# Kernel optimization log

Measured on AMD Instinct MI355X. Metric: run time of the kernel, lower is better.

Reference implementation:

```python
import jax, jax.numpy as jnp
import numpy as np
import math

B, NX, NY = 4, 64, 64
IN_DIM, OUT_DIM = 3, 3
DIM, DEPTH, HEADS, DH, FF_MULT = 192, 6, 8, 64, 4
INNER = HEADS * DH              # 512
FF = DIM * FF_MULT              # 768
M = int(DH * math.log(DH))      # 266 random features (performer default)
GROUPS = 8
LATENT_STEPS = 1
EPS_SN, EPS_K, EPS_GN = 1e-5, 1e-4, 1e-5


def setup_inputs() -> dict:
    rng = np.random.default_rng(0)
    f = lambda *s: jnp.asarray(rng.standard_normal(s).astype(np.float32) * 0.02)
    # unitary forward operator (SVD-whitened in torch == orthogonal matrix)
    Q, _ = np.linalg.qr(rng.standard_normal((DIM, DIM)).astype(np.float32))
    return {
        "x": jnp.asarray(rng.standard_normal((B, NX, NY, IN_DIM)).astype(np.float32)),
        "to_in_w": f(DIM, IN_DIM), "to_in_b": f(DIM),
        "pos_emb": f(1, NX * NY, DIM),
        "proj": jnp.asarray(rng.standard_normal((DEPTH, M, DH)).astype(np.float32)),
        "sn_attn_g": jnp.ones((DEPTH,), jnp.float32),
        "wq": f(DEPTH, INNER, DIM), "wk": f(DEPTH, INNER, DIM), "wv": f(DEPTH, INNER, DIM),
        "wo": f(DEPTH, DIM, INNER), "bo": f(DEPTH, DIM),
        "sn_ff_g": jnp.ones((DEPTH,), jnp.float32),
        "w1": f(DEPTH, FF, DIM), "b1": f(DEPTH, FF),
        "w2": f(DEPTH, DIM, FF), "b2": f(DEPTH, DIM),
        "expand_w": f(DIM, DIM),
        "fwd_w": jnp.asarray(Q.astype(np.float32)),
        "dec_lin_w": f(DIM, DIM), "dec_lin_b": f(DIM),
        "gn_g": jnp.ones((DIM,), jnp.float32), "gn_b": jnp.zeros((DIM,), jnp.float32),
        "c9_w": f(DIM, DIM // GROUPS, 9, 9), "c9_b": f(DIM),
        "c7_w": f(DIM // 2, DIM // GROUPS, 7, 7), "c7_b": f(DIM // 2),
        "c5_w": f(DIM // 4, (DIM // 2) // GROUPS, 5, 5), "c5_b": f(DIM // 4),
        "c1_w": f(OUT_DIM, DIM // 4, 1, 1), "c1_b": f(OUT_DIM),
        "latent_steps": LATENT_STEPS,
    }


def _scalenorm(x, g):
    n = jnp.linalg.norm(x, axis=-1, keepdims=True) * (x.shape[-1] ** -0.5)
    return x / jnp.maximum(n, EPS_SN) * g


def _softmax_features(data, proj, is_query):
    # data: [b,h,n,d]; proj: [m,d] -> FAVOR+ softmax-kernel features [b,h,n,m]
    dn = data.shape[-1] ** -0.25
    ratio = proj.shape[0] ** -0.5
    dd = jnp.einsum('bhnd,md->bhnm', data * dn, proj)
    diag = 0.5 * jnp.sum(data * data, -1) * (dn * dn)  # [b,h,n]
    if is_query:
        mx = jnp.max(dd, axis=-1, keepdims=True)
    else:
        mx = jnp.max(dd, axis=(-1, -2), keepdims=True)
    return ratio * (jnp.exp(dd - diag[..., None] - mx) + EPS_K)


def _attn(x, proj, wq, wk, wv, wo, bo):
    b, n, _ = x.shape
    split = lambda t: t.reshape(b, n, HEADS, DH).transpose(0, 2, 1, 3)
    q = split(x @ wq.T); k = split(x @ wk.T); v = split(x @ wv.T)
    qp = _softmax_features(q, proj, True)
    kp = _softmax_features(k, proj, False)
    context = jnp.einsum('bhnm,bhnd->bhmd', kp, v)            # [b,h,m,d]
    denom = jnp.einsum('bhnm,bhm->bhn', qp, kp.sum(2))
    out = jnp.einsum('bhnm,bhmd->bhnd', qp, context) / denom[..., None]
    out = out.transpose(0, 2, 1, 3).reshape(b, n, INNER)
    return out @ wo.T + bo


def _circ_conv(x, w, b, groups):
    p = w.shape[-1] // 2
    x = jnp.pad(x, ((0, 0), (0, 0), (p, p), (p, p)), mode='wrap')
    y = jax.lax.conv_general_dilated(x, w, (1, 1), 'VALID',
        dimension_numbers=('NCHW', 'OIHW', 'NCHW'), feature_group_count=groups)
    return y + b[None, :, None, None]


def _group_norm(x, g, b):
    B_, C, H, W = x.shape
    xg = x.reshape(B_, GROUPS, C // GROUPS, H, W)
    mu = xg.mean((2, 3, 4), keepdims=True)
    var = xg.var((2, 3, 4), keepdims=True)
    xn = ((xg - mu) * jax.lax.rsqrt(var + EPS_GN)).reshape(B_, C, H, W)
    return xn * g[None, :, None, None] + b[None, :, None, None]


def reference(x, to_in_w, to_in_b, pos_emb, proj, sn_attn_g, wq, wk, wv, wo, bo,
              sn_ff_g, w1, b1, w2, b2, expand_w, fwd_w, dec_lin_w, dec_lin_b,
              gn_g, gn_b, c9_w, c9_b, c7_w, c7_b, c5_w, c5_b, c1_w, c1_b, latent_steps):
    b, nx, ny, _ = x.shape
    h = x @ to_in_w.T + to_in_b                       # [b,nx,ny,dim]
    h = h.reshape(b, nx * ny, DIM) + pos_emb[:, :nx * ny]
    for i in range(DEPTH):                             # Performer: prenorm attn + prenorm FF
        h = h + _attn(_scalenorm(h, sn_attn_g[i]), proj[i], wq[i], wk[i], wv[i], wo[i], bo[i])
        hn = _scalenorm(h, sn_ff_g[i])
        h = h + (jax.nn.gelu(hn @ w1[i].T + b1[i], approximate=False) @ w2[i].T + b2[i])
    h = h.reshape(b, nx, ny, DIM) @ expand_w.T        # expand_latent (no bias)
    u, us = h, []
    for _ in range(latent_steps):
        u = u @ fwd_w.T                               # unitary forward operator
        us.append(u)
    u = jnp.concatenate(us, 0)                        # [(b*t), nx, ny, c]
    y = u @ dec_lin_w.T + dec_lin_b
    y = y.transpose(0, 3, 1, 2)                       # NCHW
    y = _group_norm(y, gn_g, gn_b)
    y = jax.nn.gelu(_circ_conv(y, c9_w, c9_b, GROUPS), approximate=False)
    y = jax.nn.gelu(_circ_conv(y, c7_w, c7_b, GROUPS), approximate=False)
    y = jax.nn.gelu(_circ_conv(y, c5_w, c5_b, GROUPS), approximate=False)
    y = jax.lax.conv_general_dilated(y, c1_w, (1, 1), 'VALID',
        dimension_numbers=('NCHW', 'OIHW', 'NCHW')) + c1_b[None, :, None, None]
    # einops '(b t) c nx ny -> b t nx ny c'
    y = y.reshape(b, latent_steps, OUT_DIM, nx, ny).transpose(0, 1, 3, 4, 2)
    return y
```

## Files before the change

### kernel.cpp

```cpp
#include <hip/hip_runtime.h>
#include <cmath>

#define NB      4
#define NTOK    4096
#define BNTOK   16384
#define CDIM    192
#define CINNER  512
#define NHEADS  8
#define DHEAD   64
#define CFF     768
#define MFEAT   266
#define NDEPTH  6

#define DN      0.35355339059327373f
#define RATIO   0.06131393394849658f

typedef unsigned short u16;
typedef __attribute__((ext_vector_type(8))) short s16x8;
typedef __attribute__((ext_vector_type(8))) u16  u16x8;
typedef __attribute__((ext_vector_type(4))) float f32x4;

#define OFF_H    0ull
#define OFF_HN   3145728ull
#define OFF_Q    6291456ull
#define OFF_K    14680064ull
#define OFF_V    23068672ull
#define OFF_BIG  31457280ull
#define OFF_PJ   44040192ull
#define OFF_CTXT 44163072ull
#define OFF_KMAX 47368192ull
#define OFF_GNP  47368448ull
#define OFF_GNS  47369472ull
#define OFF_WHI  47370240ull
#define OFF_WLO  49489920ull
#define WOFF_QKV 0ull
#define WOFF_WO  1769472ull
#define WOFF_W1  2359296ull
#define WOFF_W2  3244032ull
#define WOFF_EXP 4128768ull
#define WOFF_FWD 4165632ull
#define WOFF_DEC 4202496ull

#define PJL      20480
#define CTXTN    819200

__device__ __forceinline__ float gelu_f(float x) {
    return 0.5f * x * (1.0f + erff(x * 0.7071067811865476f));
}
__device__ __forceinline__ unsigned f2ord(float f) {
    int i = __float_as_int(f);
    return (i >= 0) ? ((unsigned)i | 0x80000000u) : (unsigned)(~i);
}
__device__ __forceinline__ float ord2f(unsigned u) {
    int i = (u & 0x80000000u) ? (int)(u & 0x7fffffffu) : ~(int)u;
    return __int_as_float(i);
}
__device__ __forceinline__ void split_bf16(float a, u16& h, u16& l) {
    unsigned ua = __float_as_uint(a);
    unsigned rh = (ua + 0x7FFFu + ((ua >> 16) & 1u)) >> 16;
    h = (u16)rh;
    float hf = __uint_as_float(rh << 16);
    float lo = a - hf;
    unsigned ul = __float_as_uint(lo);
    unsigned rl = (ul + 0x7FFFu + ((ul >> 16) & 1u)) >> 16;
    l = (u16)rl;
}
__device__ __forceinline__ u16 hi_bf16(float a) {
    unsigned ua = __float_as_uint(a);
    return (u16)((ua + 0x7FFFu + ((ua >> 16) & 1u)) >> 16);
}

__global__ __launch_bounds__(256) void cvt_qkv(const float* __restrict__ wq,
    const float* __restrict__ wk, const float* __restrict__ wv,
    u16* __restrict__ hi, u16* __restrict__ lo)
{
    int idx = blockIdx.x * 256 + threadIdx.x;
    int l = idx / 294912, rem = idx - l * 294912;
    int r = rem / 192, c = rem - r * 192;
    float v;
    if (r < 512)       v = wq[((size_t)l * 512 + r) * 192 + c];
    else if (r < 1024) v = wk[((size_t)l * 512 + (r - 512)) * 192 + c];
    else               v = wv[((size_t)l * 512 + (r - 1024)) * 192 + c];
    u16 h, lw; split_bf16(v, h, lw);
    hi[idx] = h; lo[idx] = lw;
}

__global__ __launch_bounds__(256) void cvt_w(const float* __restrict__ src,
    u16* __restrict__ hi, u16* __restrict__ lo, int n)
{
    int idx = blockIdx.x * 256 + threadIdx.x;
    if (idx < n) {
        u16 h, l; split_bf16(src[idx], h, l);
        hi[idx] = h; lo[idx] = l;
    }
}

__global__ __launch_bounds__(256) void cvt_dec(const float* __restrict__ e,
    const float* __restrict__ f, const float* __restrict__ d,
    u16* __restrict__ hi, u16* __restrict__ lo)
{
    int idx = blockIdx.x * 256 + threadIdx.x;
    if (idx >= 110592) return;
    int which = idx / 36864, rem = idx - which * 36864;
    float v = (which == 0) ? e[rem] : (which == 1) ? f[rem] : d[rem];
    u16 h, l; split_bf16(v, h, l);
    hi[idx] = h; lo[idx] = l;
}

__global__ __launch_bounds__(256) void cvt_pj(const float* __restrict__ proj,
    u16* __restrict__ hi, u16* __restrict__ lo)
{
    int idx = blockIdx.x * 256 + threadIdx.x;
    int l = idx / PJL, rem = idx - l * PJL;
    int m = rem >> 6, k = rem & 63;
    float v = (m < MFEAT) ? proj[(size_t)l * MFEAT * DHEAD + m * 64 + k] : 0.f;
    u16 h, lw; split_bf16(v, h, lw);
    hi[idx] = h; lo[idx] = lw;
}

__global__ __launch_bounds__(256) void input_embed(const float* __restrict__ x,
    const float* __restrict__ w, const float* __restrict__ bvec,
    const float* __restrict__ pos, float* __restrict__ h)
{
    int idx = blockIdx.x * 256 + threadIdx.x;
    int row = idx / CDIM, c = idx - row * CDIM;
    int p = row & (NTOK - 1);
    const float* xr = x + (size_t)row * 3;
    h[idx] = xr[0]*w[c*3+0] + xr[1]*w[c*3+1] + xr[2]*w[c*3+2] + bvec[c] + pos[(size_t)p*CDIM + c];
}

__global__ __launch_bounds__(256) void rownorm_kernel(const float* __restrict__ in,
    float* __restrict__ sv, const float* __restrict__ gptr, int gidx)
{
    int wv = threadIdx.x >> 6, lane = threadIdx.x & 63;
    int row = blockIdx.x * 4 + wv;
    const float* p = in + (size_t)row * CDIM;
    float x0 = p[lane], x1 = p[lane + 64], x2 = p[lane + 128];
    float ss = x0*x0 + x1*x1 + x2*x2;
    #pragma unroll
    for (int off = 32; off; off >>= 1) ss += __shfl_xor(ss, off);
    if (lane == 0) {
        float g = gptr[gidx];
        float n = sqrtf(ss * (1.0f / 192.0f));
        sv[row] = g / fmaxf(n, 1e-5f);
    }
}

#define LP 40
__global__ __launch_bounds__(256) void gemm_mfma(const float* __restrict__ A,
    const float* __restrict__ ascale,
    const u16* __restrict__ Bhi, const u16* __restrict__ Blo,
    const float* __restrict__ bias, const float* __restrict__ resid,
    float* __restrict__ C, int M, int N, int K, int epi)
{
    __shared__ u16 a_hi[128 * LP], a_lo[128 * LP], b_hi[128 * LP], b_lo[128 * LP];
    const int tid = threadIdx.x;
    const int n0 = blockIdx.x * 128, m0 = blockIdx.y * 128;
    const int wave = tid >> 6, lane = tid & 63;
    const int wr = wave >> 1, wc = wave & 1;
    const int fr = lane & 15, q = lane >> 4;
    const bool wactive = (n0 + wc * 64) < N;
    f32x4 acc[4][4];
    #pragma unroll
    for (int i = 0; i < 4; ++i)
        #pragma unroll
        for (int j = 0; j < 4; ++j) { acc[i][j][0]=0.f; acc[i][j][1]=0.f; acc[i][j][2]=0.f; acc[i][j][3]=0.f; }

    const int srow = tid >> 1, sc0 = (tid & 1) * 16;
    const float* aptr = A + (size_t)(m0 + srow) * K + sc0;
    const float as = ascale ? ascale[m0 + srow] : 1.0f;
    const bool bval = (n0 + srow) < N;
    const u16* bhp = Bhi + (size_t)(n0 + srow) * K + sc0;
    const u16* blp = Blo + (size_t)(n0 + srow) * K + sc0;
    const int soff = srow * LP + sc0;
    const int aoffb = (wr * 64 + fr) * LP + q * 8;
    const int boffb = (wc * 64 + fr) * LP + q * 8;

    for (int kc = 0; kc < K; kc += 32) {
        float4 f0 = *(const float4*)(aptr + kc);
        float4 f1 = *(const float4*)(aptr + kc + 4);
        float4 f2 = *(const float4*)(aptr + kc + 8);
        float4 f3 = *(const float4*)(aptr + kc + 12);
        u16x8 h0, l0, h1, l1;
        {
            float v[16] = {f0.x,f0.y,f0.z,f0.w, f1.x,f1.y,f1.z,f1.w,
                           f2.x,f2.y,f2.z,f2.w, f3.x,f3.y,f3.z,f3.w};
            u16 hh[16], ll[16];
            #pragma unroll
            for (int i = 0; i < 16; ++i) { float sv = v[i] * as; split_bf16(sv, hh[i], ll[i]); }
            #pragma unroll
            for (int i = 0; i < 8; ++i) { h0[i]=hh[i]; l0[i]=ll[i]; h1[i]=hh[8+i]; l1[i]=ll[8+i]; }
        }
        *(u16x8*)&a_hi[soff]     = h0;  *(u16x8*)&a_hi[soff + 8] = h1;
        *(u16x8*)&a_lo[soff]     = l0;  *(u16x8*)&a_lo[soff + 8] = l1;
        u16x8 bh0 = (u16x8)0, bh1 = (u16x8)0, bl0 = (u16x8)0, bl1 = (u16x8)0;
        if (bval) {
            bh0 = *(const u16x8*)(bhp + kc);  bh1 = *(const u16x8*)(bhp + kc + 8);
            bl0 = *(const u16x8*)(blp + kc);  bl1 = *(const u16x8*)(blp + kc + 8);
        }
        *(u16x8*)&b_hi[soff]     = bh0;  *(u16x8*)&b_hi[soff + 8] = bh1;
        *(u16x8*)&b_lo[soff]     = bl0;  *(u16x8*)&b_lo[soff + 8] = bl1;
        __syncthreads();
        if (wactive) {
            s16x8 Ah[4], Al[4], Bh[4], Bl[4];
            #pragma unroll
            for (int t = 0; t < 4; ++t) {
                Ah[t] = *(const s16x8*)&a_hi[aoffb + t * 16 * LP];
                Al[t] = *(const s16x8*)&a_lo[aoffb + t * 16 * LP];
                Bh[t] = *(const s16x8*)&b_hi[boffb + t * 16 * LP];
                Bl[t] = *(const s16x8*)&b_lo[boffb + t * 16 * LP];
            }
            #pragma unroll
            for (int i = 0; i < 4; ++i)
                #pragma unroll
                for (int j = 0; j < 4; ++j)
                    acc[i][j] = __builtin_amdgcn_mfma_f32_16x16x32_bf16(Ah[i], Bh[j], acc[i][j], 0, 0, 0);
            #pragma unroll
            for (int i = 0; i < 4; ++i)
                #pragma unroll
                for (int j = 0; j < 4; ++j)
                    acc[i][j] = __builtin_amdgcn_mfma_f32_16x16x32_bf16(Ah[i], Bl[j], acc[i][j], 0, 0, 0);
            #pragma unroll
            for (int i = 0; i < 4; ++i)
                #pragma unroll
                for (int j = 0; j < 4; ++j)
                    acc[i][j] = __builtin_amdgcn_mfma_f32_16x16x32_bf16(Al[i], Bh[j], acc[i][j], 0, 0, 0);
        }
        __syncthreads();
    }
    const int c0 = n0 + wc * 64;
    const int rowb = m0 + wr * 64;
    #pragma unroll
    for (int j = 0; j < 4; ++j) {
        int c = c0 + j * 16 + fr;
        if (c >= N) continue;
        float bb = (epi & 1) ? bias[c] : 0.f;
        float* cp;
        if (epi & 8) cp = C + (size_t)(c >> 9) * 8388608ull + (size_t)(c & 511);
        else         cp = C + c;
        const float* rp = (epi & 4) ? (resid + c) : nullptr;
        #pragma unroll
        for (int i = 0; i < 4; ++i) {
            #pragma unroll
            for (int r = 0; r < 4; ++r) {
                int row = rowb + i * 16 + q * 4 + r;
                float val = acc[i][j][r] + bb;
                if (epi & 2) val = gelu_f(val);
                if (epi & 4) val += rp[(size_t)row * N];
                size_t off = (epi & 8) ? (size_t)row * 512 : (size_t)row * N;
                cp[off] = val;
            }
        }
    }
}

__global__ void kmax_init(unsigned* kmaxu) {
    if (threadIdx.x < NDEPTH * 32) kmaxu[threadIdx.x] = 0u;
}

__global__ __launch_bounds__(256) void kmax2_kernel(const float* __restrict__ Km,
    const u16* __restrict__ pjh, unsigned* __restrict__ kmaxu)
{
    __shared__ __align__(16) u16 khi[64 * 72];
    __shared__ float wred[4];
    const int tid = threadIdx.x;
    const int nt = blockIdx.x, bh = blockIdx.y;
    const int b = bh >> 3, hh = bh & 7;
    const int wave = tid >> 6, lane = tid & 63;
    const int fr = lane & 15, quad = lane >> 4;
    float lm = -1e30f;
    const size_t kbase = ((size_t)b * NTOK) * CINNER + hh * DHEAD;
    for (int ch = 0; ch < 4; ++ch) {
        const int n0 = nt * 256 + ch * 64;
        __syncthreads();
        {
            int tok = tid >> 2, koff = (tid & 3) * 16;
            const float* kp = Km + kbase + (size_t)(n0 + tok) * CINNER + koff;
            u16 hh16[16];
            #pragma unroll
            for (int qd = 0; qd < 4; ++qd) {
                float4 f = *(const float4*)(kp + qd * 4);
                hh16[qd*4+0] = hi_bf16(f.x * DN); hh16[qd*4+1] = hi_bf16(f.y * DN);
                hh16[qd*4+2] = hi_bf16(f.z * DN); hh16[qd*4+3] = hi_bf16(f.w * DN);
            }
            u16x8 v0, v1;
            #pragma unroll
            for (int i = 0; i < 8; ++i) { v0[i] = hh16[i]; v1[i] = hh16[8+i]; }
            *(u16x8*)&khi[tok * 72 + koff] = v0;
            *(u16x8*)&khi[tok * 72 + koff + 8] = v1;
        }
        __syncthreads();
        int rowA = (wave * 16 + fr) * 72;
        s16x8 A0 = *(const s16x8*)&khi[rowA + quad * 8];
        s16x8 A1 = *(const s16x8*)&khi[rowA + 32 + quad * 8];
        for (int ct = 0; ct < 17; ++ct) {
            const u16* bp = pjh + (ct * 16 + fr) * 64 + quad * 8;
            s16x8 B0 = *(const s16x8*)bp;
            s16x8 B1 = *(const s16x8*)(bp + 32);
            f32x4 t; t[0]=0.f; t[1]=0.f; t[2]=0.f; t[3]=0.f;
            t = __builtin_amdgcn_mfma_f32_16x16x32_bf16(A0, B0, t, 0, 0, 0);
            t = __builtin_amdgcn_mfma_f32_16x16x32_bf16(A1, B1, t, 0, 0, 0);
            if (ct * 16 + fr < MFEAT) {
                #pragma unroll
                for (int r = 0; r < 4; ++r) lm = fmaxf(lm, t[r]);
            }
        }
    }
    #pragma unroll
    for (int off = 32; off; off >>= 1) lm = fmaxf(lm, __shfl_xor(lm, off));
    if (lane == 0) wred[wave] = lm;
    __syncthreads();
    if (tid == 0) {
        float m = fmaxf(fmaxf(wred[0], wred[1]), fmaxf(wred[2], wred[3]));
        atomicMax(kmaxu + bh, f2ord(m));
    }
}

__global__ __launch_bounds__(256) void ctx2_kernel(const float* __restrict__ Km,
    const float* __restrict__ Vm, const u16* __restrict__ pjh, const u16* __restrict__ pjl,
    const unsigned* __restrict__ kmaxu, float* __restrict__ part)
{
    __shared__ __align__(16) u16 khi[32 * 72], klo[32 * 72];
    __shared__ __align__(16) u16 vth[80 * 40], vtl[80 * 40];
    __shared__ __align__(16) u16 kph[4][16 * 40], kpl[4][16 * 40];
    __shared__ float diag[32];
    const int tid = threadIdx.x;
    const int bh = blockIdx.x, seg = blockIdx.y;
    const int b = bh >> 3, hh = bh & 7;
    const int wave = tid >> 6, lane = tid & 63;
    const int fr = lane & 15, quad = lane >> 4;
    const float kmx = ord2f(kmaxu[bh]);
    for (int i = tid; i < 16 * 40; i += 256) {
        int row = 64 + i / 40, col = i - (i / 40) * 40;
// ... 30 lines not shown
            #pragma unroll
            for (int i = 0; i < 8; ++i) {
                u16 h, l; split_bf16(vv[i], h, l);
                vth[(koff + i) * 40 + tok] = h;
                vtl[(koff + i) * 40 + tok] = l;
            }
        }
        __syncthreads();
        s16x8 Ah[2][2], Al[2][2];
        #pragma unroll
        for (int rt = 0; rt < 2; ++rt) {
            int rowA = (rt * 16 + fr) * 72;
            Ah[rt][0] = *(const s16x8*)&khi[rowA + quad * 8];
            Ah[rt][1] = *(const s16x8*)&khi[rowA + 32 + quad * 8];
            Al[rt][0] = *(const s16x8*)&klo[rowA + quad * 8];
            Al[rt][1] = *(const s16x8*)&klo[rowA + 32 + quad * 8];
        }
        for (int mc = 0; mc < 5; ++mc) {
            const int ct = mc * 4 + wave;
            const u16* bph = pjh + (ct * 16 + fr) * 64 + quad * 8;
            const u16* bpl = pjl + (ct * 16 + fr) * 64 + quad * 8;
            s16x8 B0h = *(const s16x8*)bph, B1h = *(const s16x8*)(bph + 32);
            s16x8 B0l = *(const s16x8*)bpl, B1l = *(const s16x8*)(bpl + 32);
            const bool valid = (ct * 16 + fr) < MFEAT;
            #pragma unroll
            for (int rt = 0; rt < 2; ++rt) {
                f32x4 dd; dd[0]=0.f; dd[1]=0.f; dd[2]=0.f; dd[3]=0.f;
                dd = __builtin_amdgcn_mfma_f32_16x16x32_bf16(Ah[rt][0], B0h, dd, 0, 0, 0);
                dd = __builtin_amdgcn_mfma_f32_16x16x32_bf16(Ah[rt][0], B0l, dd, 0, 0, 0);
                dd = __builtin_amdgcn_mfma_f32_16x16x32_bf16(Al[rt][0], B0h, dd, 0, 0, 0);
                dd = __builtin_amdgcn_mfma_f32_16x16x32_bf16(Ah[rt][1], B1h, dd, 0, 0, 0);
                dd = __builtin_amdgcn_mfma_f32_16x16x32_bf16(Ah[rt][1], B1l, dd, 0, 0, 0);
                dd = __builtin_amdgcn_mfma_f32_16x16x32_bf16(Al[rt][1], B1h, dd, 0, 0, 0);
                ushort4 ph, pl;
                #pragma unroll
                for (int r = 0; r < 4; ++r) {
                    float dgv = diag[rt * 16 + quad * 4 + r];
                    float val = valid ? RATIO * (expf(dd[r] - dgv - kmx) + 1e-4f) : 0.f;
                    u16 h, l; split_bf16(val, h, l);
                    (&ph.x)[r] = h; (&pl.x)[r] = l;
                }
                *(ushort4*)&sh[fr * 40 + rt * 16 + quad * 4] = ph;
                *(ushort4*)&sl[fr * 40 + rt * 16 + quad * 4] = pl;
            }
            s16x8 Bh = *(const s16x8*)&sh[fr * 40 + quad * 8];
            s16x8 Bl = *(const s16x8*)&sl[fr * 40 + quad * 8];
            #pragma unroll
            for (int rt2 = 0; rt2 < 5; ++rt2) {
                s16x8 Vh = *(const s16x8*)&vth[(rt2 * 16 + fr) * 40 + quad * 8];
                s16x8 Vl = *(const s16x8*)&vtl[(rt2 * 16 + fr) * 40 + quad * 8];
                accv[rt2][mc] = __builtin_amdgcn_mfma_f32_16x16x32_bf16(Vh, Bh, accv[rt2][mc], 0, 0, 0);
                accv[rt2][mc] = __builtin_amdgcn_mfma_f32_16x16x32_bf16(Vh, Bl, accv[rt2][mc], 0, 0, 0);
                accv[rt2][mc] = __builtin_amdgcn_mfma_f32_16x16x32_bf16(Vl, Bh, accv[rt2][mc], 0, 0, 0);
            }
        }
    }
    float* pb = part + ((size_t)(seg * 32 + bh)) * 80 * 320;
    #pragma unroll
    for (int rt2 = 0; rt2 < 5; ++rt2) {
        #pragma unroll
        for (int mc = 0; mc < 5; ++mc) {
            int ct = mc * 4 + wave;
            #pragma unroll
            for (int r = 0; r < 4; ++r)
                pb[(size_t)(rt2 * 16 + quad * 4 + r) * 320 + ct * 16 + fr] = accv[rt2][mc][r];
        }
    }
}

__global__ __launch_bounds__(256) void ctxt_reduce(const float* __restrict__ part,
    u16* __restrict__ cth, u16* __restrict__ ctl)
{
    int idx = blockIdx.x * 256 + threadIdx.x;
    float s = 0.f;
    #pragma unroll
    for (int sg = 0; sg < 8; ++sg) s += part[(size_t)sg * CTXTN + idx];
    u16 h, l; split_bf16(s, h, l);
    cth[idx] = h; ctl[idx] = l;
}

__global__ __launch_bounds__(256) void qside2_kernel(const float* __restrict__ Qm,
    const u16* __restrict__ pjh, const u16* __restrict__ pjl,
    const u16* __restrict__ cth, const u16* __restrict__ ctl,
    float* __restrict__ attn_out)
{
    __shared__ __align__(16) u16 qhi[64 * 72], qlo[64 * 72];
    __shared__ __align__(16) u16 slabh[4][16 * 72], slabl[4][16 * 72];
    __shared__ float diag[64];
    const int tid = threadIdx.x;
    const int nt = blockIdx.x, bh = blockIdx.y;
    const int b = bh >> 3, hh = bh & 7;
    const int wave = tid >> 6, lane = tid & 63;
    const int fr = lane & 15, quad = lane >> 4;
    const int n0 = nt * 64;
    {
        int tok = tid >> 2, koff = (tid & 3) * 16;
        const float* qp = Qm + ((size_t)(b * NTOK + n0 + tok)) * CINNER + hh * DHEAD + koff;
        float v[16]; float ps = 0.f;
        #pragma unroll
        for (int qd = 0; qd < 4; ++qd) {
            float4 f = *(const float4*)(qp + qd * 4);
            v[qd*4+0]=f.x*DN; v[qd*4+1]=f.y*DN; v[qd*4+2]=f.z*DN; v[qd*4+3]=f.w*DN;
        }
        u16x8 h0, l0, h1, l1;
        #pragma unroll
        for (int i = 0; i < 8; ++i) {
            u16 h, l; split_bf16(v[i], h, l); h0[i]=h; l0[i]=l;
            split_bf16(v[8+i], h, l); h1[i]=h; l1[i]=l;
        }
        #pragma unroll
        for (int i = 0; i < 16; ++i) ps += v[i]*v[i];
        *(u16x8*)&qhi[tok * 72 + koff] = h0;  *(u16x8*)&qhi[tok * 72 + koff + 8] = h1;
        *(u16x8*)&qlo[tok * 72 + koff] = l0;  *(u16x8*)&qlo[tok * 72 + koff + 8] = l1;
        ps += __shfl_xor(ps, 1); ps += __shfl_xor(ps, 2);
        if ((tid & 3) == 0) diag[tok] = 0.5f * ps;
    }
    __syncthreads();
    f32x4 dd[20];
    #pragma unroll
    for (int ct = 0; ct < 20; ++ct) { dd[ct][0]=0.f; dd[ct][1]=0.f; dd[ct][2]=0.f; dd[ct][3]=0.f; }
    {
        int rowA = (wave * 16 + fr) * 72;
        s16x8 A0h = *(const s16x8*)&qhi[rowA + quad * 8];
        s16x8 A1h = *(const s16x8*)&qhi[rowA + 32 + quad * 8];
        s16x8 A0l = *(const s16x8*)&qlo[rowA + quad * 8];
        s16x8 A1l = *(const s16x8*)&qlo[rowA + 32 + quad * 8];
        #pragma unroll
        for (int ct = 0; ct < 20; ++ct) {
            const u16* bph = pjh + (ct * 16 + fr) * 64 + quad * 8;
            const u16* bpl = pjl + (ct * 16 + fr) * 64 + quad * 8;
            s16x8 B0h = *(const s16x8*)bph, B1h = *(const s16x8*)(bph + 32);
            s16x8 B0l = *(const s16x8*)bpl, B1l = *(const s16x8*)(bpl + 32);
            dd[ct] = __builtin_amdgcn_mfma_f32_16x16x32_bf16(A0h, B0h, dd[ct], 0, 0, 0);
            dd[ct] = __builtin_amdgcn_mfma_f32_16x16x32_bf16(A0h, B0l, dd[ct], 0, 0, 0);
            dd[ct] = __builtin_amdgcn_mfma_f32_16x16x32_bf16(A0l, B0h, dd[ct], 0, 0, 0);
            dd[ct] = __builtin_amdgcn_mfma_f32_16x16x32_bf16(A1h, B1h, dd[ct], 0, 0, 0);
            dd[ct] = __builtin_amdgcn_mfma_f32_16x16x32_bf16(A1h, B1l, dd[ct], 0, 0, 0);
            dd[ct] = __builtin_amdgcn_mfma_f32_16x16x32_bf16(A1l, B1h, dd[ct], 0, 0, 0);
        }
    }
    float pm[4] = {-1e30f, -1e30f, -1e30f, -1e30f};
    #pragma unroll
    for (int ct = 0; ct < 20; ++ct) {
        if (ct * 16 + fr < MFEAT) {
            #pragma unroll
            for (int r = 0; r < 4; ++r) pm[r] = fmaxf(pm[r], dd[ct][r]);
        }
    }
    #pragma unroll
    for (int r = 0; r < 4; ++r) {
        pm[r] = fmaxf(pm[r], __shfl_xor(pm[r], 1));
        pm[r] = fmaxf(pm[r], __shfl_xor(pm[r], 2));
        pm[r] = fmaxf(pm[r], __shfl_xor(pm[r], 4));
        pm[r] = fmaxf(pm[r], __shfl_xor(pm[r], 8));
    }
    float dg[4];
    #pragma unroll
    for (int r = 0; r < 4; ++r) dg[r] = diag[wave * 16 + quad * 4 + r];
    #pragma unroll
    for (int ct = 0; ct < 20; ++ct) {
        bool valid = (ct * 16 + fr) < MFEAT;
        #pragma unroll
        for (int r = 0; r < 4; ++r)
            dd[ct][r] = valid ? RATIO * (expf(dd[ct][r] - dg[r] - pm[r]) + 1e-4f) : 0.f;
    }
    f32x4 acc[5];
    #pragma unroll
    for (int dt = 0; dt < 5; ++dt) { acc[dt][0]=0.f; acc[dt][1]=0.f; acc[dt][2]=0.f; acc[dt][3]=0.f; }
    u16* sh = slabh[wave];  u16* sl = slabl[wave];
    for (int mc = 0; mc < 5; ++mc) {
        #pragma unroll
        for (int c = 0; c < 4; ++c) {
            int ct = mc * 4 + c;
            #pragma unroll
            for (int r = 0; r < 4; ++r) {
                u16 h, l; split_bf16(dd[ct][r], h, l);
                int tok = quad * 4 + r;
                sh[tok * 72 + c * 16 + fr] = h;
                sl[tok * 72 + c * 16 + fr] = l;
            }
        }
        #pragma unroll
        for (int ks = 0; ks < 2; ++ks) {
            s16x8 Ah = *(const s16x8*)&sh[fr * 72 + ks * 32 + quad * 8];
            s16x8 Al = *(const s16x8*)&sl[fr * 72 + ks * 32 + quad * 8];
            #pragma unroll
            for (int dt = 0; dt < 5; ++dt) {
                const u16* bph = cth + ((size_t)bh * 80 + dt * 16 + fr) * 320 + mc * 64 + ks * 32 + quad * 8;
                const u16* bpl = ctl + ((size_t)bh * 80 + dt * 16 + fr) * 320 + mc * 64 + ks * 32 + quad * 8;
                s16x8 Bh = *(const s16x8*)bph;
                s16x8 Bl = *(const s16x8*)bpl;
                acc[dt] = __builtin_amdgcn_mfma_f32_16x16x32_bf16(Ah, Bh, acc[dt], 0, 0, 0);
                acc[dt] = __builtin_amdgcn_mfma_f32_16x16x32_bf16(Ah, Bl, acc[dt], 0, 0, 0);
                acc[dt] = __builtin_amdgcn_mfma_f32_16x16x32_bf16(Al, Bh, acc[dt], 0, 0, 0);
            }
        }
    }
    #pragma unroll
    for (int r = 0; r < 4; ++r) {
        float denom = __shfl(acc[4][r], lane & 48);
        float inv = 1.0f / denom;
        int token = n0 + wave * 16 + quad * 4 + r;
        float* op = attn_out + ((size_t)(b * NTOK + token)) * CINNER + hh * DHEAD;
        #pragma unroll
        for (int dt = 0; dt < 4; ++dt)
            op[dt * 16 + fr] = acc[dt][r] * inv;
    }
}

__global__ __launch_bounds__(256) void gn_part_kernel(const float* __restrict__ y,
    float2* __restrict__ part)
{
    __shared__ float s_s[256], s_q[256];
    const int tid = threadIdx.x;
    const int sp = blockIdx.x, g = blockIdx.y, b = blockIdx.z;
    int p = sp * 256 + tid;
    const float* base = y + ((size_t)(b * NTOK + p)) * CDIM + g * 24;
    float s = 0.f, q = 0.f;
    #pragma unroll
    for (int i = 0; i < 24; ++i) { float v = base[i]; s += v; q += v * v; }
    s_s[tid] = s; s_q[tid] = q;
    __syncthreads();
    for (int st = 128; st; st >>= 1) {
        if (tid < st) { s_s[tid] += s_s[tid + st]; s_q[tid] += s_q[tid + st]; }
        __syncthreads();
    }
    if (tid == 0) part[(b * 8 + g) * 16 + sp] = make_float2(s_s[0], s_q[0]);
}

__global__ void gn_stat_kernel(const float2* __restrict__ part, float2* __restrict__ stat)
{
    int bg = threadIdx.x;
    if (bg < 32) {
        float s = 0.f, q = 0.f;
        for (int i = 0; i < 16; ++i) { float2 v = part[bg * 16 + i]; s += v.x; q += v.y; }
        float mean = s * (1.0f / 98304.0f);
        float var = q * (1.0f / 98304.0f) - mean * mean;
        stat[bg] = make_float2(mean, rsqrtf(var + 1e-5f));
    }
}

__global__ __launch_bounds__(256) void gn_apply_kernel(const float* __restrict__ y,
    const float2* __restrict__ stat, const float* __restrict__ gg,
    const float* __restrict__ gb, float* __restrict__ out)
{
    __shared__ float tile[64][65];
    const int tid = threadIdx.x;
    const int pt = blockIdx.x, ct = blockIdx.y, b = blockIdx.z;
    const int p0 = pt * 64, c0 = ct * 64;
    #pragma unroll
    for (int r = 0; r < 4; ++r) {
        int id = tid + r * 256;
        int pr = id >> 4, kq = (id & 15) * 4;
        float4 v = *(const float4*)(y + ((size_t)(b * NTOK + p0 + pr)) * CDIM + c0 + kq);
        tile[pr][kq+0] = v.x; tile[pr][kq+1] = v.y; tile[pr][kq+2] = v.z; tile[pr][kq+3] = v.w;
    }
    __syncthreads();
    const int cc = tid >> 6, pp = tid & 63;
    #pragma unroll
    for (int i = 0; i < 16; ++i) {
        int c = c0 + cc * 16 + i;
        int g = c / 24;
        float2 st = stat[b * 8 + g];
        float v = tile[pp][cc * 16 + i];
        out[((size_t)(b * CDIM + c)) * NTOK + p0 + pp] = (v - st.x) * st.y * gg[c] + gb[c];
    }
}

template<int KS, int CIN, int COUT, int OX, int YS, int OCB>
__global__ __launch_bounds__(256) void circ_conv3(const float* __restrict__ in,
    const float* __restrict__ w, const float* __restrict__ bias,
    float* __restrict__ out, int do_gelu)
{
    constexpr int P   = KS / 2;
    constexpr int ICG = CIN / 8;
    constexpr int OCG = COUT / 8;
    constexpr int TW  = 64 + 2 * P;
    constexpr int TR  = 64 / YS + 2 * P;
    constexpr int RS0 = (TW + 3) & ~3;
    constexpr int RS  = (RS0 % 8 == 0) ? RS0 + 4 : RS0;
    constexpr int TCX = 64 / OX;
    constexpr int RV  = (OX + KS - 1 + 3) & ~3;
    constexpr int NLD = (TR * TW + 255) / 256;
    __shared__ __align__(16) float tile[TR * RS];
    const int tid = threadIdx.x;
    const int oc0 = blockIdx.x * OCB;
    const int y0  = blockIdx.y * (64 / YS);
    const int b   = blockIdx.z;
    const int g   = oc0 / OCG;
    const int tx  = tid % TCX, ty = tid / TCX;
    int srcs[NLD], dsts[NLD];
    #pragma unroll
    for (int j = 0; j < NLD; ++j) {
        int idx = tid + j * 256;
        if (idx < TR * TW) {
            int r = idx / TW, c = idx - r * TW;
            int gy = (y0 + r - P) & 63, gx = (c - P) & 63;
            srcs[j] = gy * 64 + gx;
            dsts[j] = r * RS + c;
        } else { srcs[j] = 0; dsts[j] = -1; }
    }
    float acc[OCB][OX] = {};
    const float* ip0 = in + ((size_t)(b * CIN + g * ICG)) * 4096;
    #pragma unroll 1
    for (int ic = 0; ic < ICG; ++ic) {
        __syncthreads();
        const float* ip = ip0 + (size_t)ic * 4096;
        #pragma unroll
        for (int j = 0; j < NLD; ++j)
            if (dsts[j] >= 0) tile[dsts[j]] = ip[srcs[j]];
        __syncthreads();
        const float* wp = w + ((size_t)oc0 * ICG + ic) * (KS * KS);
        #pragma unroll 1
        for (int ky = 0; ky < KS; ++ky) {
            float wreg[OCB][KS];
            #pragma unroll
            for (int oc = 0; oc < OCB; ++oc)
                #pragma unroll
                for (int kx = 0; kx < KS; ++kx)
                    wreg[oc][kx] = wp[(size_t)oc * ICG * KS * KS + ky * KS + kx];
            float rv[RV];
            const float* rp = &tile[(ty + ky) * RS + tx * OX];
            #pragma unroll
            for (int q2 = 0; q2 < RV / 4; ++q2)
                *(float4*)&rv[q2 * 4] = *(const float4*)(rp + q2 * 4);
            #pragma unroll
            for (int kx = 0; kx < KS; ++kx)
                #pragma unroll
                for (int oc = 0; oc < OCB; ++oc)
                    #pragma unroll
                    for (int ox = 0; ox < OX; ++ox)
                        acc[oc][ox] += rv[kx + ox] * wreg[oc][kx];
        }
    }
    const int y = y0 + ty, x = tx * OX;
    #pragma unroll
    for (int oc = 0; oc < OCB; ++oc) {
        float bv = bias[oc0 + oc];
        float vo[OX];
        #pragma unroll
        for (int ox = 0; ox < OX; ++ox) {
            float vv = acc[oc][ox] + bv;
            vo[ox] = do_gelu ? gelu_f(vv) : vv;
        }
        float* op = out + (((size_t)(b * COUT + oc0 + oc) * 64 + y)) * 64 + x;
        #pragma unroll
        for (int q2 = 0; q2 < OX / 4; ++q2)
            *(float4*)(op + q2 * 4) = *(float4*)&vo[q2 * 4];
    }
}

__global__ __launch_bounds__(256) void conv1_kernel(const float* __restrict__ in,
    const float* __restrict__ w, const float* __restrict__ bias, float* __restrict__ out)
{
    int idx = blockIdx.x * 256 + threadIdx.x;
    int b = idx >> 12, p = idx & 4095;
    float a0 = bias[0], a1 = bias[1], a2 = bias[2];
    const float* ip = in + (size_t)b * 48 * NTOK + p;
    #pragma unroll 8
    for (int ic = 0; ic < 48; ++ic) {
        float v = ip[(size_t)ic * NTOK];
        a0 += v * w[ic]; a1 += v * w[48 + ic]; a2 += v * w[96 + ic];
    }
    float* op = out + (size_t)idx * 3;
    op[0] = a0; op[1] = a1; op[2] = a2;
}

static inline void gemm_mf(hipStream_t s, const float* A, const float* ascale,
                           const u16* Bhi, const u16* Blo,
                           const float* bias, const float* resid, float* C,
                           int M, int N, int K, int epi)
{
    dim3 g((N + 127) / 128, M / 128);
    hipLaunchKernelGGL(gemm_mfma, g, dim3(256), 0, s, A, ascale, Bhi, Blo, bias, resid, C, M, N, K, epi);
}

extern "C" void kernel_launch(void* const* d_in, const int* in_sizes, int n_in,
                              void* d_out, int out_size, void* d_ws, size_t ws_size,
                              hipStream_t stream)
{
    (void)in_sizes; (void)n_in; (void)out_size; (void)ws_size;
    const float* x        = (const float*)d_in[0];
    const float* to_in_w  = (const float*)d_in[1];
    const float* to_in_b  = (const float*)d_in[2];
    const float* pos_emb  = (const float*)d_in[3];
    const float* proj     = (const float*)d_in[4];
    const float* sn_attn_g= (const float*)d_in[5];
    const float* wq       = (const float*)d_in[6];
    const float* wk       = (const float*)d_in[7];
    const float* wv       = (const float*)d_in[8];
    const float* wo       = (const float*)d_in[9];
    const float* bo       = (const float*)d_in[10];
    const float* sn_ff_g  = (const float*)d_in[11];
    const float* w1       = (const float*)d_in[12];
    const float* b1       = (const float*)d_in[13];
    const float* w2       = (const float*)d_in[14];
    const float* b2       = (const float*)d_in[15];
    const float* expand_w = (const float*)d_in[16];
    const float* fwd_w    = (const float*)d_in[17];
    const float* dec_lin_w= (const float*)d_in[18];
    const float* dec_lin_b= (const float*)d_in[19];
    const float* gn_g     = (const float*)d_in[20];
    const float* gn_b     = (const float*)d_in[21];
    const float* c9_w     = (const float*)d_in[22];
    const float* c9_b     = (const float*)d_in[23];
    const float* c7_w     = (const float*)d_in[24];
    const float* c7_b     = (const float*)d_in[25];
    const float* c5_w     = (const float*)d_in[26];
    const float* c5_b     = (const float*)d_in[27];
    const float* c1_w     = (const float*)d_in[28];
    const float* c1_b     = (const float*)d_in[29];
    float* out = (float*)d_out;

    float* ws = (float*)d_ws;
    float* h   = ws + OFF_H;
    float* hn  = ws + OFF_HN;
    float* sbuf = ws + OFF_HN;
    float* q   = ws + OFF_Q;
    float* k   = ws + OFF_K;
    float* v   = ws + OFF_V;
    float* big = ws + OFF_BIG;
    u16* pjhi = (u16*)(ws + OFF_PJ);
    u16* pjlo = pjhi + 6 * PJL;
    u16* cthi = (u16*)(ws + OFF_CTXT);
    u16* ctlo = cthi + CTXTN;
    unsigned* kmaxu = (unsigned*)(ws + OFF_KMAX);
    float2* gnp = (float2*)(ws + OFF_GNP);
    float2* gns = (float2*)(ws + OFF_GNS);
    u16* whi = (u16*)(ws + OFF_WHI);
    u16* wlo = (u16*)(ws + OFF_WLO);

    hipLaunchKernelGGL(input_embed, dim3(BNTOK * CDIM / 256), dim3(256), 0, stream,
                       x, to_in_w, to_in_b, pos_emb, h);
    hipLaunchKernelGGL(kmax_init, dim3(1), dim3(256), 0, stream, kmaxu);
    hipLaunchKernelGGL(cvt_qkv, dim3(6912), dim3(256), 0, stream, wq, wk, wv,
                       whi + WOFF_QKV, wlo + WOFF_QKV);
    hipLaunchKernelGGL(cvt_w, dim3(2304), dim3(256), 0, stream, wo, whi + WOFF_WO, wlo + WOFF_WO, 589824);
    hipLaunchKernelGGL(cvt_w, dim3(3456), dim3(256), 0, stream, w1, whi + WOFF_W1, wlo + WOFF_W1, 884736);
    hipLaunchKernelGGL(cvt_w, dim3(3456), dim3(256), 0, stream, w2, whi + WOFF_W2, wlo + WOFF_W2, 884736);
    hipLaunchKernelGGL(cvt_dec, dim3(432), dim3(256), 0, stream, expand_w, fwd_w, dec_lin_w,
                       whi + WOFF_EXP, wlo + WOFF_EXP);
    hipLaunchKernelGGL(cvt_pj, dim3(480), dim3(256), 0, stream, proj, pjhi, pjlo);

    for (int l = 0; l < NDEPTH; ++l) {
        const float* bo_l = bo + (size_t)l * CDIM;
        const float* b1_l = b1 + (size_t)l * CFF;
        const float* b2_l = b2 + (size_t)l * CDIM;
        const u16* pjh_l = pjhi + (size_t)l * PJL;
        const u16* pjl_l = pjlo + (size_t)l * PJL;
        unsigned* kmax_l = kmaxu + l * 32;

        hipLaunchKernelGGL(rownorm_kernel, dim3(BNTOK / 4), dim3(256), 0, stream, h, sbuf, sn_attn_g, l);
        gemm_mf(stream, h, sbuf, whi + WOFF_QKV + (size_t)l * 294912, wlo + WOFF_QKV + (size_t)l * 294912,
                nullptr, nullptr, q, BNTOK, 1536, CDIM, 8);
        hipLaunchKernelGGL(kmax2_kernel, dim3(16, 32), dim3(256), 0, stream, k, pjh_l, kmax_l);
        hipLaunchKernelGGL(ctx2_kernel, dim3(32, 8), dim3(256), 0, stream, k, v, pjh_l, pjl_l, kmax_l, big);
        hipLaunchKernelGGL(ctxt_reduce, dim3(CTXTN / 256), dim3(256), 0, stream, big, cthi, ctlo);
        hipLaunchKernelGGL(qside2_kernel, dim3(64, 32), dim3(256), 0, stream, q, pjh_l, pjl_l, cthi, ctlo, k);
        gemm_mf(stream, k, nullptr, whi + WOFF_WO + (size_t)l * 98304, wlo + WOFF_WO + (size_t)l * 98304,
                bo_l, h, h, BNTOK, CDIM, CINNER, 1 | 4);

        hipLaunchKernelGGL(rownorm_kernel, dim3(BNTOK / 4), dim3(256), 0, stream, h, sbuf, sn_ff_g, l);
        gemm_mf(stream, h, sbuf, whi + WOFF_W1 + (size_t)l * 147456, wlo + WOFF_W1 + (size_t)l * 147456,
                b1_l, nullptr, big, BNTOK, CFF, CDIM, 1 | 2);
        gemm_mf(stream, big, nullptr, whi + WOFF_W2 + (size_t)l * 147456, wlo + WOFF_W2 + (size_t)l * 147456,
                b2_l, h, h, BNTOK, CDIM, CFF, 1 | 4);
    }

    gemm_mf(stream, h, nullptr, whi + WOFF_EXP, wlo + WOFF_EXP, nullptr, nullptr, hn, BNTOK, CDIM, CDIM, 0);
    gemm_mf(stream, hn, nullptr, whi + WOFF_FWD, wlo + WOFF_FWD, nullptr, nullptr, h, BNTOK, CDIM, CDIM, 0);
    gemm_mf(stream, h, nullptr, whi + WOFF_DEC, wlo + WOFF_DEC, dec_lin_b, nullptr, hn, BNTOK, CDIM, CDIM, 1);

    float* y0 = big;
    float* y1 = big + 3145728;
    float* y2 = big + 6291456;
    float* y3 = big + 7864320;
    hipLaunchKernelGGL(gn_part_kernel, dim3(16, 8, 4), dim3(256), 0, stream, hn, gnp);
    hipLaunchKernelGGL(gn_stat_kernel, dim3(1), dim3(32), 0, stream, gnp, gns);
    hipLaunchKernelGGL(gn_apply_kernel, dim3(64, 3, 4), dim3(256), 0, stream, hn, gns, gn_g, gn_b, y0);

    hipLaunchKernelGGL((circ_conv3<9, 192, 192, 8, 2, 3>), dim3(64, 2, 4), dim3(256), 0, stream,
                       y0, c9_w, c9_b, y1, 1);
    hipLaunchKernelGGL((circ_conv3<7, 192, 96, 8, 2, 3>), dim3(32, 2, 4), dim3(256), 0, stream,
                       y1, c7_w, c7_b, y2, 1);
    hipLaunchKernelGGL((circ_conv3<5, 96, 48, 4, 4, 3>), dim3(16, 4, 4), dim3(256), 0, stream,
                       y2, c5_w, c5_b, y3, 1);
    hipLaunchKernelGGL(conv1_kernel, dim3(BNTOK / 256), dim3(256), 0, stream, y3, c1_w, c1_b, out);
}
```

Baseline: 3.613 ms.

## Store activations as pre-split bf16 hi/lo pairs and apply row scale in epilogue

Activations that feed the GEMMs (residual stream, attention output, FF hidden, decoder intermediates) are now stored as bf16 hi/lo pairs, so the GEMM A-tile loader copies them straight into shared memory instead of loading fp32 and splitting each element. The ScaleNorm row scale moves from the A-load path to the GEMM epilogue, where it multiplies the accumulator. This removes the repeated per-tile split arithmetic and keeps the activation traffic the same size, since two bf16 values take the same bytes as one fp32. In exchange the epilogues and the rownorm kernel split or recombine pairs, and the workspace layout is remapped, which adds aliasing risk.

```diff
diff --git a/kernel.cpp b/kernel.cpp
--- a/kernel.cpp
+++ b/kernel.cpp
@@ -28,6 +28,7 @@
 #define OFF_BIG  31457280ull
 #define OFF_PJ   44040192ull
 #define OFF_CTXT 44163072ull
+#define OFF_SB   44982272ull
 #define OFF_KMAX 47368192ull
 #define OFF_GNP  47368448ull
 #define OFF_GNS  47369472ull
@@ -44,6 +45,13 @@
 #define PJL      20480
 #define CTXTN    819200
 
+#define EP_BIAS  1
+#define EP_GELU  2
+#define EP_RESID 4
+#define EP_QKV   8
+#define EP_SROW  16
+#define EP_PAIR  32
+
 __device__ __forceinline__ float gelu_f(float x) {
     return 0.5f * x * (1.0f + erff(x * 0.7071067811865476f));
 }
@@ -69,6 +77,9 @@
     unsigned ua = __float_as_uint(a);
     return (u16)((ua + 0x7FFFu + ((ua >> 16) & 1u)) >> 16);
 }
+__device__ __forceinline__ float bf2f(u16 u) {
+    return __uint_as_float(((unsigned)u) << 16);
+}
 
 __global__ __launch_bounds__(256) void cvt_qkv(const float* __restrict__ wq,
     const float* __restrict__ wk, const float* __restrict__ wv,
@@ -120,22 +131,27 @@
 
 __global__ __launch_bounds__(256) void input_embed(const float* __restrict__ x,
     const float* __restrict__ w, const float* __restrict__ bvec,
-    const float* __restrict__ pos, float* __restrict__ h)
+    const float* __restrict__ pos, u16* __restrict__ hhi, u16* __restrict__ hlo)
 {
     int idx = blockIdx.x * 256 + threadIdx.x;
     int row = idx / CDIM, c = idx - row * CDIM;
     int p = row & (NTOK - 1);
     const float* xr = x + (size_t)row * 3;
-    h[idx] = xr[0]*w[c*3+0] + xr[1]*w[c*3+1] + xr[2]*w[c*3+2] + bvec[c] + pos[(size_t)p*CDIM + c];
-}
-
-__global__ __launch_bounds__(256) void rownorm_kernel(const float* __restrict__ in,
-    float* __restrict__ sv, const float* __restrict__ gptr, int gidx)
+    float val = xr[0]*w[c*3+0] + xr[1]*w[c*3+1] + xr[2]*w[c*3+2] + bvec[c] + pos[(size_t)p*CDIM + c];
+    u16 h, l; split_bf16(val, h, l);
+    hhi[idx] = h; hlo[idx] = l;
+}
+
+__global__ __launch_bounds__(256) void rownorm_kernel(const u16* __restrict__ hhi,
+    const u16* __restrict__ hlo, float* __restrict__ sv,
+    const float* __restrict__ gptr, int gidx)
 {
     int wv = threadIdx.x >> 6, lane = threadIdx.x & 63;
     int row = blockIdx.x * 4 + wv;
-    const float* p = in + (size_t)row * CDIM;
-    float x0 = p[lane], x1 = p[lane + 64], x2 = p[lane + 128];
+    size_t base = (size_t)row * CDIM;
+    float x0 = bf2f(hhi[base + lane]) + bf2f(hlo[base + lane]);
+    float x1 = bf2f(hhi[base + lane + 64]) + bf2f(hlo[base + lane + 64]);
+    float x2 = bf2f(hhi[base + lane + 128]) + bf2f(hlo[base + lane + 128]);
     float ss = x0*x0 + x1*x1 + x2*x2;
     #pragma unroll
     for (int off = 32; off; off >>= 1) ss += __shfl_xor(ss, off);
@@ -147,11 +163,14 @@
 }
 
 #define LP 40
-__global__ __launch_bounds__(256) void gemm_mfma(const float* __restrict__ A,
-    const float* __restrict__ ascale,
+__global__ __launch_bounds__(256) void gemm_mfma(
+    const u16* __restrict__ Ahi, const u16* __restrict__ Alo,
+    const float* __restrict__ srow,
     const u16* __restrict__ Bhi, const u16* __restrict__ Blo,
-    const float* __restrict__ bias, const float* __restrict__ resid,
-    float* __restrict__ C, int M, int N, int K, int epi)
+    const float* __restrict__ bias,
+    const u16* __restrict__ Rhi, const u16* __restrict__ Rlo,
+    float* __restrict__ Cf, u16* __restrict__ Chi, u16* __restrict__ Clo,
+    int M, int N, int K, int epi)
 {
     __shared__ u16 a_hi[128 * LP], a_lo[128 * LP], b_hi[128 * LP], b_lo[128 * LP];
     const int tid = threadIdx.x;
@@ -166,33 +185,21 @@
         #pragma unroll
         for (int j = 0; j < 4; ++j) { acc[i][j][0]=0.f; acc[i][j][1]=0.f; acc[i][j][2]=0.f; acc[i][j][3]=0.f; }
 
-    const int srow = tid >> 1, sc0 = (tid & 1) * 16;
-    const float* aptr = A + (size_t)(m0 + srow) * K + sc0;
-    const float as = ascale ? ascale[m0 + srow] : 1.0f;
-    const bool bval = (n0 + srow) < N;
-    const u16* bhp = Bhi + (size_t)(n0 + srow) * K + sc0;
-    const u16* blp = Blo + (size_t)(n0 + srow) * K + sc0;
-    const int soff = srow * LP + sc0;
+    const int srw = tid >> 1, sc0 = (tid & 1) * 16;
+    const u16* ahp = Ahi + (size_t)(m0 + srw) * K + sc0;
+    const u16* alp = Alo + (size_t)(m0 + srw) * K + sc0;
+    const bool bval = (n0 + srw) < N;
+    const u16* bhp = Bhi + (size_t)(n0 + srw) * K + sc0;
+    const u16* blp = Blo + (size_t)(n0 + srw) * K + sc0;
+    const int soff = srw * LP + sc0;
     const int aoffb = (wr * 64 + fr) * LP + q * 8;
     const int boffb = (wc * 64 + fr) * LP + q * 8;
 
     for (int kc = 0; kc < K; kc += 32) {
-        float4 f0 = *(const float4*)(aptr + kc);
-        float4 f1 = *(const float4*)(aptr + kc + 4);
-        float4 f2 = *(const float4*)(aptr + kc + 8);
-        float4 f3 = *(const float4*)(aptr + kc + 12);
-        u16x8 h0, l0, h1, l1;
-        {
-            float v[16] = {f0.x,f0.y,f0.z,f0.w, f1.x,f1.y,f1.z,f1.w,
-                           f2.x,f2.y,f2.z,f2.w, f3.x,f3.y,f3.z,f3.w};
-            u16 hh[16], ll[16];
-            #pragma unroll
-            for (int i = 0; i < 16; ++i) { float sv = v[i] * as; split_bf16(sv, hh[i], ll[i]); }
-            #pragma unroll
-            for (int i = 0; i < 8; ++i) { h0[i]=hh[i]; l0[i]=ll[i]; h1[i]=hh[8+i]; l1[i]=ll[8+i]; }
-        }
-        *(u16x8*)&a_hi[soff]     = h0;  *(u16x8*)&a_hi[soff + 8] = h1;
-        *(u16x8*)&a_lo[soff]     = l0;  *(u16x8*)&a_lo[soff + 8] = l1;
+        *(u16x8*)&a_hi[soff]     = *(const u16x8*)(ahp + kc);
+        *(u16x8*)&a_hi[soff + 8] = *(const u16x8*)(ahp + kc + 8);
+        *(u16x8*)&a_lo[soff]     = *(const u16x8*)(alp + kc);
+        *(u16x8*)&a_lo[soff + 8] = *(const u16x8*)(alp + kc + 8);
         u16x8 bh0 = (u16x8)0, bh1 = (u16x8)0, bl0 = (u16x8)0, bl1 = (u16x8)0;
         if (bval) {
             bh0 = *(const u16x8*)(bhp + kc);  bh1 = *(const u16x8*)(bhp + kc + 8);
@@ -230,25 +237,38 @@
     }
     const int c0 = n0 + wc * 64;
     const int rowb = m0 + wr * 64;
+    float sv[4][4];
+    if (epi & EP_SROW) {
+        #pragma unroll
+        for (int i = 0; i < 4; ++i)
+            #pragma unroll
+            for (int r = 0; r < 4; ++r)
+                sv[i][r] = srow[rowb + i * 16 + q * 4 + r];
+    }
     #pragma unroll
     for (int j = 0; j < 4; ++j) {
         int c = c0 + j * 16 + fr;
         if (c >= N) continue;
-        float bb = (epi & 1) ? bias[c] : 0.f;
-        float* cp;
-        if (epi & 8) cp = C + (size_t)(c >> 9) * 8388608ull + (size_t)(c & 511);
-        else         cp = C + c;
-        const float* rp = (epi & 4) ? (resid + c) : nullptr;
+        float bb = (epi & EP_BIAS) ? bias[c] : 0.f;
         #pragma unroll
         for (int i = 0; i < 4; ++i) {
             #pragma unroll
             for (int r = 0; r < 4; ++r) {
                 int row = rowb + i * 16 + q * 4 + r;
-                float val = acc[i][j][r] + bb;
-                if (epi & 2) val = gelu_f(val);
-                if (epi & 4) val += rp[(size_t)row * N];
-                size_t off = (epi & 8) ? (size_t)row * 512 : (size_t)row * N;
-                cp[off] = val;
+                float val = acc[i][j][r];
+                if (epi & EP_SROW) val *= sv[i][r];
+                val += bb;
+                if (epi & EP_GELU) val = gelu_f(val);
+                size_t off = (size_t)row * N + c;
+                if (epi & EP_RESID) val += bf2f(Rhi[off]) + bf2f(Rlo[off]);
+                if (epi & EP_QKV) {
+                    Cf[(size_t)(c >> 9) * 8388608ull + (size_t)row * 512 + (size_t)(c & 511)] = val;
+                } else if (epi & EP_PAIR) {
+                    u16 hh2, ll2; split_bf16(val, hh2, ll2);
+                    Chi[off] = hh2; Clo[off] = ll2;
+                } else {
+                    Cf[off] = val;
+                }
             }
         }
     }
@@ -445,7 +465,7 @@
 __global__ __launch_bounds__(256) void qside2_kernel(const float* __restrict__ Qm,
     const u16* __restrict__ pjh, const u16* __restrict__ pjl,
     const u16* __restrict__ cth, const u16* __restrict__ ctl,
-    float* __restrict__ attn_out)
+    u16* __restrict__ ahi, u16* __restrict__ alo)
 {
     __shared__ __align__(16) u16 qhi[64 * 72], qlo[64 * 72];
     __shared__ __align__(16) u16 slabh[4][16 * 72], slabl[4][16 * 72];
@@ -564,10 +584,13 @@
         float denom = __shfl(acc[4][r], lane & 48);
         float inv = 1.0f / denom;
         int token = n0 + wave * 16 + quad * 4 + r;
-        float* op = attn_out + ((size_t)(b * NTOK + token)) * CINNER + hh * DHEAD;
-        #pragma unroll
-        for (int dt = 0; dt < 4; ++dt)
-            op[dt * 16 + fr] = acc[dt][r] * inv;
+        size_t obase = ((size_t)(b * NTOK + token)) * CINNER + hh * DHEAD;
+        #pragma unroll
+        for (int dt = 0; dt < 4; ++dt) {
+            u16 h2, l2; split_bf16(acc[dt][r] * inv, h2, l2);
+            ahi[obase + dt * 16 + fr] = h2;
+            alo[obase + dt * 16 + fr] = l2;
+        }
     }
 }
 
@@ -729,13 +752,15 @@
     op[0] = a0; op[1] = a1; op[2] = a2;
 }
 
-static inline void gemm_mf(hipStream_t s, const float* A, const float* ascale,
-                           const u16* Bhi, const u16* Blo,
-                           const float* bias, const float* resid, float* C,
+static inline void gemm_mf(hipStream_t s, const u16* Ahi, const u16* Alo, const float* srow,
+                           const u16* Bhi, const u16* Blo, const float* bias,
+                           const u16* Rhi, const u16* Rlo,
+                           float* Cf, u16* Chi, u16* Clo,
                            int M, int N, int K, int epi)
 {
     dim3 g((N + 127) / 128, M / 128);
-    hipLaunchKernelGGL(gemm_mfma, g, dim3(256), 0, s, A, ascale, Bhi, Blo, bias, resid, C, M, N, K, epi);
+    hipLaunchKernelGGL(gemm_mfma, g, dim3(256), 0, s, Ahi, Alo, srow, Bhi, Blo, bias,
+                       Rhi, Rlo, Cf, Chi, Clo, M, N, K, epi);
 }
 
 extern "C" void kernel_launch(void* const* d_in, const int* in_sizes, int n_in,
@@ -776,17 +801,23 @@
     float* out = (float*)d_out;
 
     float* ws = (float*)d_ws;
-    float* h   = ws + OFF_H;
-    float* hn  = ws + OFF_HN;
-    float* sbuf = ws + OFF_HN;
+    u16* hhi = (u16*)(ws + OFF_H);
+    u16* hlo = hhi + 3145728;
+    u16* ehi = (u16*)(ws + OFF_HN);
+    u16* elo = ehi + 3145728;
     float* q   = ws + OFF_Q;
     float* k   = ws + OFF_K;
+    u16* ahi = (u16*)(ws + OFF_K);
+    u16* alo = ahi + 8388608;
     float* v   = ws + OFF_V;
     float* big = ws + OFF_BIG;
+    u16* bhi = (u16*)(ws + OFF_BIG);
+    u16* blo = bhi + 12582912;
     u16* pjhi = (u16*)(ws + OFF_PJ);
     u16* pjlo = pjhi + 6 * PJL;
     u16* cthi = (u16*)(ws + OFF_CTXT);
     u16* ctlo = cthi + CTXTN;
+    float* sbuf = ws + OFF_SB;
     unsigned* kmaxu = (unsigned*)(ws + OFF_KMAX);
     float2* gnp = (float2*)(ws + OFF_GNP);
     float2* gns = (float2*)(ws + OFF_GNS);
@@ -794,7 +825,7 @@
     u16* wlo = (u16*)(ws + OFF_WLO);
 
     hipLaunchKernelGGL(input_embed, dim3(BNTOK * CDIM / 256), dim3(256), 0, stream,
-                       x, to_in_w, to_in_b, pos_emb, h);
+                       x, to_in_w, to_in_b, pos_emb, hhi, hlo);
     hipLaunchKernelGGL(kmax_init, dim3(1), dim3(256), 0, stream, kmaxu);
     hipLaunchKernelGGL(cvt_qkv, dim3(6912), dim3(256), 0, stream, wq, wk, wv,
                        whi + WOFF_QKV, wlo + WOFF_QKV);
@@ -813,34 +844,46 @@
         const u16* pjl_l = pjlo + (size_t)l * PJL;
         unsigned* kmax_l = kmaxu + l * 32;
 
-        hipLaunchKernelGGL(rownorm_kernel, dim3(BNTOK / 4), dim3(256), 0, stream, h, sbuf, sn_attn_g, l);
-        gemm_mf(stream, h, sbuf, whi + WOFF_QKV + (size_t)l * 294912, wlo + WOFF_QKV + (size_t)l * 294912,
-                nullptr, nullptr, q, BNTOK, 1536, CDIM, 8);
+        hipLaunchKernelGGL(rownorm_kernel, dim3(BNTOK / 4), dim3(256), 0, stream, hhi, hlo, sbuf, sn_attn_g, l);
+        gemm_mf(stream, hhi, hlo, sbuf,
+                whi + WOFF_QKV + (size_t)l * 294912, wlo + WOFF_QKV + (size_t)l * 294912,
+                nullptr, nullptr, nullptr, q, nullptr, nullptr,
+                BNTOK, 1536, CDIM, EP_QKV | EP_SROW);
         hipLaunchKernelGGL(kmax2_kernel, dim3(16, 32), dim3(256), 0, stream, k, pjh_l, kmax_l);
         hipLaunchKernelGGL(ctx2_kernel, dim3(32, 8), dim3(256), 0, stream, k, v, pjh_l, pjl_l, kmax_l, big);
         hipLaunchKernelGGL(ctxt_reduce, dim3(CTXTN / 256), dim3(256), 0, stream, big, cthi, ctlo);
-        hipLaunchKernelGGL(qside2_kernel, dim3(64, 32), dim3(256), 0, stream, q, pjh_l, pjl_l, cthi, ctlo, k);
-        gemm_mf(stream, k, nullptr, whi + WOFF_WO + (size_t)l * 98304, wlo + WOFF_WO + (size_t)l * 98304,
-                bo_l, h, h, BNTOK, CDIM, CINNER, 1 | 4);
-
-        hipLaunchKernelGGL(rownorm_kernel, dim3(BNTOK / 4), dim3(256), 0, stream, h, sbuf, sn_ff_g, l);
-        gemm_mf(stream, h, sbuf, whi + WOFF_W1 + (size_t)l * 147456, wlo + WOFF_W1 + (size_t)l * 147456,
-                b1_l, nullptr, big, BNTOK, CFF, CDIM, 1 | 2);
-        gemm_mf(stream, big, nullptr, whi + WOFF_W2 + (size_t)l * 147456, wlo + WOFF_W2 + (size_t)l * 147456,
-                b2_l, h, h, BNTOK, CDIM, CFF, 1 | 4);
-    }
-
-    gemm_mf(stream, h, nullptr, whi + WOFF_EXP, wlo + WOFF_EXP, nullptr, nullptr, hn, BNTOK, CDIM, CDIM, 0);
-    gemm_mf(stream, hn, nullptr, whi + WOFF_FWD, wlo + WOFF_FWD, nullptr, nullptr, h, BNTOK, CDIM, CDIM, 0);
-    gemm_mf(stream, h, nullptr, whi + WOFF_DEC, wlo + WOFF_DEC, dec_lin_b, nullptr, hn, BNTOK, CDIM, CDIM, 1);
+        hipLaunchKernelGGL(qside2_kernel, dim3(64, 32), dim3(256), 0, stream, q, pjh_l, pjl_l, cthi, ctlo,
+                           ahi, alo);
+        gemm_mf(stream, ahi, alo, nullptr,
+                whi + WOFF_WO + (size_t)l * 98304, wlo + WOFF_WO + (size_t)l * 98304,
+                bo_l, hhi, hlo, nullptr, hhi, hlo,
+                BNTOK, CDIM, CINNER, EP_BIAS | EP_RESID | EP_PAIR);
+
+        hipLaunchKernelGGL(rownorm_kernel, dim3(BNTOK / 4), dim3(256), 0, stream, hhi, hlo, sbuf, sn_ff_g, l);
+        gemm_mf(stream, hhi, hlo, sbuf,
+                whi + WOFF_W1 + (size_t)l * 147456, wlo + WOFF_W1 + (size_t)l * 147456,
+                b1_l, nullptr, nullptr, nullptr, bhi, blo,
+                BNTOK, CFF, CDIM, EP_BIAS | EP_GELU | EP_SROW | EP_PAIR);
+        gemm_mf(stream, bhi, blo, nullptr,
+                whi + WOFF_W2 + (size_t)l * 147456, wlo + WOFF_W2 + (size_t)l * 147456,
+                b2_l, hhi, hlo, nullptr, hhi, hlo,
+                BNTOK, CDIM, CFF, EP_BIAS | EP_RESID | EP_PAIR);
+    }
+
+    gemm_mf(stream, hhi, hlo, nullptr, whi + WOFF_EXP, wlo + WOFF_EXP,
+            nullptr, nullptr, nullptr, nullptr, ehi, elo, BNTOK, CDIM, CDIM, EP_PAIR);
+    gemm_mf(stream, ehi, elo, nullptr, whi + WOFF_FWD, wlo + WOFF_FWD,
+            nullptr, nullptr, nullptr, nullptr, hhi, hlo, BNTOK, CDIM, CDIM, EP_PAIR);
+    gemm_mf(stream, hhi, hlo, nullptr, whi + WOFF_DEC, wlo + WOFF_DEC,
+            dec_lin_b, nullptr, nullptr, q, nullptr, nullptr, BNTOK, CDIM, CDIM, EP_BIAS);
 
     float* y0 = big;
     float* y1 = big + 3145728;
     float* y2 = big + 6291456;
     float* y3 = big + 7864320;
-    hipLaunchKernelGGL(gn_part_kernel, dim3(16, 8, 4), dim3(256), 0, stream, hn, gnp);
+    hipLaunchKernelGGL(gn_part_kernel, dim3(16, 8, 4), dim3(256), 0, stream, q, gnp);
     hipLaunchKernelGGL(gn_stat_kernel, dim3(1), dim3(32), 0, stream, gnp, gns);
-    hipLaunchKernelGGL(gn_apply_kernel, dim3(64, 3, 4), dim3(256), 0, stream, hn, gns, gn_g, gn_b, y0);
+    hipLaunchKernelGGL(gn_apply_kernel, dim3(64, 3, 4), dim3(256), 0, stream, q, gns, gn_g, gn_b, y0);
 
     hipLaunchKernelGGL((circ_conv3<9, 192, 192, 8, 2, 3>), dim3(64, 2, 4), dim3(256), 0, stream,
                        y0, c9_w, c9_b, y1, 1);
```

After: 3.777 ms. 1.05x slower.
